# Kernel tuning notes

Measured on AMD Instinct MI355X. Metric: run time of the kernel, lower is better.

## Reference

```python
import jax, jax.numpy as jnp
import numpy as np

E = 1024
H = 16
D = E // H  # projection_dim = 64


def setup_inputs() -> dict:
    key = jax.random.key(0)
    ks = jax.random.split(key, 9)
    s = 1.0 / np.sqrt(E)
    return {
        "inputs": jax.random.normal(ks[0], (2, 2048, E), dtype=jnp.float32),
        "Wq": jax.random.uniform(ks[1], (E, E), jnp.float32, -s, s),
        "bq": jax.random.uniform(ks[2], (E,), jnp.float32, -s, s),
        "Wk": jax.random.uniform(ks[3], (E, E), jnp.float32, -s, s),
        "bk": jax.random.uniform(ks[4], (E,), jnp.float32, -s, s),
        "Wv": jax.random.uniform(ks[5], (E, E), jnp.float32, -s, s),
        "bv": jax.random.uniform(ks[6], (E,), jnp.float32, -s, s),
        "Wo": jax.random.uniform(ks[7], (E, E), jnp.float32, -s, s),
        "bo": jax.random.uniform(ks[8], (E,), jnp.float32, -s, s),
    }


def reference(inputs, Wq, bq, Wk, bk, Wv, bv, Wo, bo):
    B, S, _ = inputs.shape
    # Linear layers use y = x @ W.T + b (torch convention); weights here stored as [E,E]
    q = inputs @ Wq.T + bq
    k = inputs @ Wk.T + bk
    v = inputs @ Wv.T + bv
    # separate heads: [B,S,E] -> [B,H,S,D]
    q = q.reshape(B, S, H, D).transpose(0, 2, 1, 3)
    k = k.reshape(B, S, H, D).transpose(0, 2, 1, 3)
    v = v.reshape(B, S, H, D).transpose(0, 2, 1, 3)
    scale = 1.0 / jnp.sqrt(jnp.float32(D))
    scores = jnp.einsum('bhqd,bhkd->bhqk', q, k) * scale  # [B,H,S,S]
    weights = jax.nn.softmax(scores, axis=-1)
    attn = jnp.einsum('bhqk,bhkd->bhqd', weights, v)  # [B,H,S,D]
    concat = attn.transpose(0, 2, 1, 3).reshape(B, S, E)
    # dropout is identity in eval mode
    return concat @ Wo.T + bo
```

## Files before the change

kernel.cpp:

```cpp
#include <hip/hip_runtime.h>
#include <hip/hip_bf16.h>
#include <stdint.h>

#define E_ 1024
#define H_ 16
#define D_ 64
#define B_ 2
#define S_ 2048
#define M_ 4096

typedef __bf16 bf16_t;
typedef __bf16 bf16x8 __attribute__((ext_vector_type(8)));
typedef __bf16 bf16x4 __attribute__((ext_vector_type(4)));
typedef __bf16 bf16x2 __attribute__((ext_vector_type(2)));
typedef float  f32x4  __attribute__((ext_vector_type(4)));
typedef float  f32x16 __attribute__((ext_vector_type(16)));
typedef unsigned int u32x2 __attribute__((ext_vector_type(2)));
typedef unsigned int u32x4 __attribute__((ext_vector_type(4)));

__global__ __launch_bounds__(256) void cvt_all(
    const float* __restrict__ x,
    const float* __restrict__ w0, const float* __restrict__ w1,
    const float* __restrict__ w2, const float* __restrict__ w3,
    bf16_t* __restrict__ xd,
    bf16_t* __restrict__ d0, bf16_t* __restrict__ d1,
    bf16_t* __restrict__ d2, bf16_t* __restrict__ d3) {
  int i = blockIdx.x * blockDim.x + threadIdx.x;
  const float* src;
  bf16_t* dst;
  int off;
  if (i < (1 << 20)) {
    src = x; dst = xd; off = i;
  } else {
    int j = i - (1 << 20);
    int z = j >> 18;
    off = j & ((1 << 18) - 1);
    src = (z == 0) ? w0 : (z == 1) ? w1 : (z == 2) ? w2 : w3;
    dst = (z == 0) ? d0 : (z == 1) ? d1 : (z == 2) ? d2 : d3;
  }
  float4 v = reinterpret_cast<const float4*>(src)[off];
  bf16x4 o;
  o[0] = (bf16_t)v.x; o[1] = (bf16_t)v.y; o[2] = (bf16_t)v.z; o[3] = (bf16_t)v.w;
  reinterpret_cast<bf16x4*>(dst)[off] = o;
}

static __device__ __forceinline__ void gl_lds16(const bf16_t* g, bf16_t* l) {
  __builtin_amdgcn_global_load_lds((__attribute__((address_space(1))) void*)g,
                                   (__attribute__((address_space(3))) void*)l,
                                   16, 0, 0);
}

template <int SWAP>
static __device__ __forceinline__ void gemm128_mainloop(
    const bf16_t* __restrict__ Ag, const bf16_t* __restrict__ Bg,
    bf16_t* ldsA0, bf16_t* ldsA1, bf16_t* ldsB0, bf16_t* ldsB1,
    int m0, int n0, f32x4 acc[4][4]) {
  const int tid  = threadIdx.x;
  const int lane = tid & 63, wave = tid >> 6;
  const int lrow = lane & 15, lgrp = lane >> 4;
  const int wr = (wave >> 1) * 64, wc = (wave & 1) * 64;
  const int skol = (lane & 3) * 8;
  const int c0 = wave * 2;
  const int rowA = c0 * 16 + (lane >> 2);
  const f32x4 zero = {0.f, 0.f, 0.f, 0.f};
#pragma unroll
  for (int i = 0; i < 4; i++)
#pragma unroll
    for (int j = 0; j < 4; j++) acc[i][j] = zero;

  gl_lds16(Ag + (size_t)(m0 + rowA) * E_ + skol,      ldsA0 + c0 * 512);
  gl_lds16(Ag + (size_t)(m0 + rowA + 16) * E_ + skol, ldsA0 + (c0 + 1) * 512);
  gl_lds16(Bg + (size_t)(n0 + rowA) * E_ + skol,      ldsB0 + c0 * 512);
  gl_lds16(Bg + (size_t)(n0 + rowA + 16) * E_ + skol, ldsB0 + (c0 + 1) * 512);
  __syncthreads();

  for (int kt = 0; kt < E_ / 32; ++kt) {
    bf16_t* sA = (kt & 1) ? ldsA1 : ldsA0;
    bf16_t* sB = (kt & 1) ? ldsB1 : ldsB0;
    if (kt + 1 < E_ / 32) {
      bf16_t* dA = (kt & 1) ? ldsA0 : ldsA1;
      bf16_t* dB = (kt & 1) ? ldsB0 : ldsB1;
      const int k0 = (kt + 1) * 32;
      gl_lds16(Ag + (size_t)(m0 + rowA) * E_ + k0 + skol,      dA + c0 * 512);
      gl_lds16(Ag + (size_t)(m0 + rowA + 16) * E_ + k0 + skol, dA + (c0 + 1) * 512);
      gl_lds16(Bg + (size_t)(n0 + rowA) * E_ + k0 + skol,      dB + c0 * 512);
      gl_lds16(Bg + (size_t)(n0 + rowA + 16) * E_ + k0 + skol, dB + (c0 + 1) * 512);
    }
    bf16x8 fA[4], fB[4];
#pragma unroll
    for (int i = 0; i < 4; i++)
      fA[i] = *reinterpret_cast<const bf16x8*>(sA + (wr + i * 16 + lrow) * 32 + lgrp * 8);
#pragma unroll
    for (int j = 0; j < 4; j++)
      fB[j] = *reinterpret_cast<const bf16x8*>(sB + (wc + j * 16 + lrow) * 32 + lgrp * 8);
#pragma unroll
    for (int i = 0; i < 4; i++)
#pragma unroll
      for (int j = 0; j < 4; j++)
        acc[i][j] = SWAP
          ? __builtin_amdgcn_mfma_f32_16x16x32_bf16(fB[j], fA[i], acc[i][j], 0, 0, 0)
          : __builtin_amdgcn_mfma_f32_16x16x32_bf16(fA[i], fB[j], acc[i][j], 0, 0, 0);
    __syncthreads();
  }
}

__global__ __launch_bounds__(256) void qkv_gemm(
    const bf16_t* __restrict__ xbf, const bf16_t* __restrict__ Wqkv,
    const float* __restrict__ bq, const float* __restrict__ bk, const float* __restrict__ bv,
    bf16_t* __restrict__ Qo, bf16_t* __restrict__ Ko, bf16_t* __restrict__ Vt) {
  __shared__ alignas(16) bf16_t ldsA[2][128 * 32];
  __shared__ alignas(16) bf16_t ldsB[2][128 * 32];
  const int m0 = blockIdx.x * 128, n0 = blockIdx.y * 128;
  const int z = n0 >> 10;
  const float* bias = (z == 0) ? bq : ((z == 1) ? bk : bv);
  const int lane = threadIdx.x & 63, wave = threadIdx.x >> 6;
  const int lrow = lane & 15, lgrp = lane >> 4;
  const int wr = (wave >> 1) * 64, wc = (wave & 1) * 64;
  f32x4 acc[4][4];

  if (z == 2) {
    gemm128_mainloop<0>(xbf, Wqkv, ldsA[0], ldsA[1], ldsB[0], ldsB[1], m0, n0, acc);
#pragma unroll
    for (int i = 0; i < 4; i++) {
      const int mbase = m0 + wr + i * 16 + lgrp * 4;
      const int b = mbase >> 11, s = mbase & (S_ - 1);
#pragma unroll
      for (int j = 0; j < 4; j++) {
        const int nl = (n0 & 1023) + wc + j * 16 + lrow;
        const float bn = bias[nl];
        const int h = nl >> 6, d = nl & 63;
        bf16x4 v;
#pragma unroll
        for (int r = 0; r < 4; r++) v[r] = (bf16_t)(acc[i][j][r] + bn);
        *reinterpret_cast<bf16x4*>(Vt + ((size_t)((b * H_ + h) * D_ + d)) * S_ + s) = v;
      }
    }
  } else {
    gemm128_mainloop<1>(xbf, Wqkv, ldsA[0], ldsA[1], ldsB[0], ldsB[1], m0, n0, acc);
    bf16_t* O = (z == 0) ? Qo : Ko;
    const float scale = (z == 0) ? 0.18033688011112042f : 1.0f;
#pragma unroll
    for (int i = 0; i < 4; i++) {
      const int m = m0 + wr + i * 16 + lrow;
      const int b = m >> 11, s = m & (S_ - 1);
#pragma unroll
      for (int j = 0; j < 4; j++) {
        const int nb = (n0 & 1023) + wc + j * 16 + lgrp * 4;
        const int h = nb >> 6, d = nb & 63;
        const f32x4 b4 = *reinterpret_cast<const f32x4*>(bias + nb);
        bf16x4 v;
#pragma unroll
        for (int r = 0; r < 4; r++) v[r] = (bf16_t)((acc[i][j][r] + b4[r]) * scale);
        *reinterpret_cast<bf16x4*>(O + ((size_t)((b * H_ + h) * S_) + s) * D_ + d) = v;
      }
    }
  }
}

__global__ __launch_bounds__(256) void out_gemm(
    const bf16_t* __restrict__ Cbf, const bf16_t* __restrict__ Wob,
    const float* __restrict__ bo, float* __restrict__ out) {
  __shared__ alignas(16) bf16_t ldsA[2][128 * 32];
  __shared__ alignas(16) bf16_t ldsB[2][128 * 32];
  const int m0 = blockIdx.x * 128, n0 = blockIdx.y * 128;
  f32x4 acc[4][4];
  gemm128_mainloop<1>(Cbf, Wob, ldsA[0], ldsA[1], ldsB[0], ldsB[1], m0, n0, acc);

  const int lane = threadIdx.x & 63, wave = threadIdx.x >> 6;
  const int lrow = lane & 15, lgrp = lane >> 4;
  const int wr = (wave >> 1) * 64, wc = (wave & 1) * 64;
#pragma unroll
  for (int i = 0; i < 4; i++) {
    const int m = m0 + wr + i * 16 + lrow;
#pragma unroll
    for (int j = 0; j < 4; j++) {
      const int nb = n0 + wc + j * 16 + lgrp * 4;
      const f32x4 b4 = *reinterpret_cast<const f32x4*>(bo + nb);
      f32x4 v = acc[i][j] + b4;
      *reinterpret_cast<f32x4*>(out + (size_t)m * E_ + nb) = v;
    }
  }
}


static __device__ __forceinline__ unsigned pack2(float a, float b) {
  bf16x2 t; t[0] = (bf16_t)a; t[1] = (bf16_t)b;
  return __builtin_bit_cast(unsigned, t);
}

static __device__ __forceinline__ bf16x8 mkfrag(unsigned a0, unsigned a1,
                                                unsigned a2, unsigned a3) {
  u32x2 s02 = __builtin_amdgcn_permlane32_swap(a0, a2, false, false);
  u32x2 s13 = __builtin_amdgcn_permlane32_swap(a1, a3, false, false);
  u32x4 t; t[0] = s02[0]; t[1] = s13[0]; t[2] = s02[1]; t[3] = s13[1];
  return *reinterpret_cast<bf16x8*>(&t);
}

__global__ __launch_bounds__(512) void attn_kernel(
    const bf16_t* __restrict__ Qg, const bf16_t* __restrict__ Kg,
    const bf16_t* __restrict__ Vtg, bf16_t* __restrict__ Og) {
  __shared__ alignas(16) bf16_t Kl[2][2][64 * 64];
  __shared__ alignas(16) bf16_t Vl[2][2][64 * 64];
  const int f = blockIdx.x;
  const int bh = (f & 7) * 4 + (f >> 7);
  const int q0 = ((f >> 3) & 15) * 128;
  const int tid = threadIdx.x, lane = tid & 63, wave = tid >> 6;
  const int qsub = wave & 3, kvg = wave >> 2;
  const int ql = lane & 31, hi = lane >> 5;
  const bf16_t* Qb = Qg + (size_t)bh * S_ * D_;
  const bf16_t* Kb = Kg + (size_t)bh * S_ * D_;
  const bf16_t* Vb = Vtg + (size_t)bh * D_ * S_;

  const int q = q0 + qsub * 32 + ql;
  bf16x8 qf[4];
#pragma unroll
  for (int ds = 0; ds < 4; ds++)
    qf[ds] = *reinterpret_cast<const bf16x8*>(Qb + (size_t)q * D_ + ds * 16 + hi * 8);

  f32x16 o0, o1;
#pragma unroll
  for (int r = 0; r < 16; r++) { o0[r] = 0.f; o1[r] = 0.f; }
  float li = 0.f;

  const int srow_lo = lane >> 3;
  const int sunit = lane & 7;

#pragma unroll
  for (int p = 0; p < 2; p++) {
    int c = p * 4 + qsub;
    int row = c * 8 + srow_lo;
    int u = sunit ^ (row & 7);
    gl_lds16(Kb + (size_t)(kvg * 64 + row) * D_ + u * 8, &Kl[kvg][0][c * 512]);
    gl_lds16(Vb + (size_t)row * S_ + kvg * 64 + u * 8, &Vl[kvg][0][c * 512]);
  }
  __syncthreads();

  for (int it = 0; it < S_ / 128; ++it) {
    const int cur = it & 1;
    if (it + 1 < S_ / 128) {
      const int kvn = (kvg + (it + 1) * 2) * 64;
#pragma unroll
      for (int p = 0; p < 2; p++) {
        int c = p * 4 + qsub;
        int row = c * 8 + srow_lo;
        int u = sunit ^ (row & 7);
        gl_lds16(Kb + (size_t)(kvn + row) * D_ + u * 8, &Kl[kvg][cur ^ 1][c * 512]);
        gl_lds16(Vb + (size_t)row * S_ + kvn + u * 8, &Vl[kvg][cur ^ 1][c * 512]);
      }
    }
    const char* kbuf = reinterpret_cast<const char*>(&Kl[kvg][cur][0]);
    const char* vbuf = reinterpret_cast<const char*>(&Vl[kvg][cur][0]);

    f32x16 pa0, pa1;
#pragma unroll
    for (int r = 0; r < 16; r++) { pa0[r] = 0.f; pa1[r] = 0.f; }
    __builtin_amdgcn_s_setprio(1);
#pragma unroll
    for (int ds = 0; ds < 4; ds++) {
      {
        const int krow = ql;
        const int u = (ds * 2 + hi) ^ (krow & 7);
        bf16x8 kf = *reinterpret_cast<const bf16x8*>(kbuf + krow * 128 + u * 16);
        pa0 = __builtin_amdgcn_mfma_f32_32x32x16_bf16(kf, qf[ds], pa0, 0, 0, 0);
      }
      {
        const int krow = 32 + ql;
        const int u = (ds * 2 + hi) ^ (krow & 7);
        bf16x8 kf = *reinterpret_cast<const bf16x8*>(kbuf + krow * 128 + u * 16);
        pa1 = __builtin_amdgcn_mfma_f32_32x32x16_bf16(kf, qf[ds], pa1, 0, 0, 0);
      }
    }
    __builtin_amdgcn_s_setprio(0);

#pragma unroll
    for (int r = 0; r < 16; r++) {
      pa0[r] = __builtin_amdgcn_exp2f(pa0[r]);
      pa1[r] = __builtin_amdgcn_exp2f(pa1[r]);
    }
    float s8[8];
#pragma unroll
    for (int i = 0; i < 8; i++)
      s8[i] = (pa0[2 * i] + pa0[2 * i + 1]) + (pa1[2 * i] + pa1[2 * i + 1]);
    float s4a = s8[0] + s8[1], s4b = s8[2] + s8[3];
    float s4c = s8[4] + s8[5], s4d = s8[6] + s8[7];
    float ps = (s4a + s4b) + (s4c + s4d);
    {
      u32x2 ss = __builtin_amdgcn_permlane32_swap(
          __builtin_bit_cast(unsigned, ps), __builtin_bit_cast(unsigned, ps), false, false);
      ps = __builtin_bit_cast(float, ss[0]) + __builtin_bit_cast(float, ss[1]);
    }
    li += ps;

    unsigned w0[8], w1[8];
#pragma unroll
    for (int i = 0; i < 8; i++) {
      w0[i] = pack2(pa0[2 * i], pa0[2 * i + 1]);
      w1[i] = pack2(pa1[2 * i], pa1[2 * i + 1]);
    }
    bf16x8 bfr[4];
    bfr[0] = mkfrag(w0[0], w0[1], w0[2], w0[3]);
    bfr[1] = mkfrag(w0[4], w0[5], w0[6], w0[7]);
    bfr[2] = mkfrag(w1[0], w1[1], w1[2], w1[3]);
    bfr[3] = mkfrag(w1[4], w1[5], w1[6], w1[7]);

    __builtin_amdgcn_s_setprio(1);
#pragma unroll
    for (int step = 0; step < 4; step++) {
      {
        const int vrow = ql;
        const int u = (step * 2 + hi) ^ (vrow & 7);
        bf16x8 vf = *reinterpret_cast<const bf16x8*>(vbuf + vrow * 128 + u * 16);
        o0 = __builtin_amdgcn_mfma_f32_32x32x16_bf16(vf, bfr[step], o0, 0, 0, 0);
      }
      {
        const int vrow = 32 + ql;
        const int u = (step * 2 + hi) ^ (vrow & 7);
        bf16x8 vf = *reinterpret_cast<const bf16x8*>(vbuf + vrow * 128 + u * 16);
        o1 = __builtin_amdgcn_mfma_f32_32x32x16_bf16(vf, bfr[step], o1, 0, 0, 0);
      }
    }
    __builtin_amdgcn_s_setprio(0);

    __syncthreads();
  }

  f32x4* smO = reinterpret_cast<f32x4*>(&Kl[0][0][0]);
  float* smL = reinterpret_cast<float*>(&Vl[0][0][0]);
  const int mi_ = qsub * 64 + lane;
  if (kvg == 1) {
#pragma unroll
    for (int g = 0; g < 4; g++) {
      f32x4 a;
#pragma unroll
      for (int i = 0; i < 4; i++) a[i] = o0[g * 4 + i];
      smO[g * 256 + mi_] = a;
    }
#pragma unroll
    for (int g = 0; g < 4; g++) {
      f32x4 a;
#pragma unroll
      for (int i = 0; i < 4; i++) a[i] = o1[g * 4 + i];
      smO[(g + 4) * 256 + mi_] = a;
    }
    smL[mi_] = li;
  }
  __syncthreads();
  if (kvg == 0) {
    li += smL[mi_];
#pragma unroll
    for (int g = 0; g < 4; g++) {
      f32x4 a = smO[g * 256 + mi_];
#pragma unroll
      for (int i = 0; i < 4; i++) o0[g * 4 + i] += a[i];
    }
#pragma unroll
    for (int g = 0; g < 4; g++) {
      f32x4 a = smO[(g + 4) * 256 + mi_];
#pragma unroll
      for (int i = 0; i < 4; i++) o1[g * 4 + i] += a[i];
    }
    const float inv = 1.0f / li;
    const int b = bh >> 4, h = bh & 15;
    bf16_t* orow = Og + (size_t)(b * S_ + q) * E_ + h * 64;
#pragma unroll
    for (int g = 0; g < 4; g++) {
      bf16x4 v;
#pragma unroll
      for (int i = 0; i < 4; i++) v[i] = (bf16_t)(o0[g * 4 + i] * inv);
      *reinterpret_cast<bf16x4*>(orow + g * 8 + hi * 4) = v;
    }
#pragma unroll
    for (int g = 0; g < 4; g++) {
      bf16x4 v;
#pragma unroll
      for (int i = 0; i < 4; i++) v[i] = (bf16_t)(o1[g * 4 + i] * inv);
      *reinterpret_cast<bf16x4*>(orow + 32 + g * 8 + hi * 4) = v;
    }
  }
}

extern "C" void kernel_launch(void* const* d_in, const int* in_sizes, int n_in,
                              void* d_out, int out_size, void* d_ws, size_t ws_size,
                              hipStream_t stream) {
  (void)in_sizes; (void)n_in; (void)out_size; (void)ws_size;
  const float* x  = (const float*)d_in[0];
  const float* Wq = (const float*)d_in[1];
  const float* bq = (const float*)d_in[2];
  const float* Wk = (const float*)d_in[3];
  const float* bk = (const float*)d_in[4];
  const float* Wv = (const float*)d_in[5];
  const float* bv = (const float*)d_in[6];
  const float* Wo = (const float*)d_in[7];
  const float* bo = (const float*)d_in[8];
  float* out = (float*)d_out;

  bf16_t* ws  = (bf16_t*)d_ws;
  bf16_t* xbf = ws;
  bf16_t* Ct  = ws;
  bf16_t* wqb = ws + (4u << 20);
  bf16_t* wkb = ws + (5u << 20);
  bf16_t* wvb = ws + (6u << 20);
  bf16_t* wob = ws + (7u << 20);
  bf16_t* Qt  = ws + (8u << 20);
  bf16_t* Kt  = ws + (12u << 20);
  bf16_t* Vt  = ws + (16u << 20);

  cvt_all<<<8192, 256, 0, stream>>>(x, Wq, Wk, Wv, Wo, xbf, wqb, wkb, wvb, wob);

  qkv_gemm<<<dim3(32, 24), 256, 0, stream>>>(xbf, wqb, bq, bk, bv, Qt, Kt, Vt);
  attn_kernel<<<512, 512, 0, stream>>>(Qt, Kt, Vt, Ct);
  out_gemm<<<dim3(32, 8), 256, 0, stream>>>(Ct, wob, bo, out);
}
```

Baseline: 128.2 us.

## Store K/V in MFMA-fragment order and load directly from global, dropping LDS staging

The QKV GEMM epilogue now writes K and V in a pre-swizzled per-lane fragment layout, so the attention kernel can load each MFMA operand with one coalesced 16-byte global load per lane. This removes the LDS double buffer, the async global-to-LDS copies and the per-iteration block barrier in the attention loop. The cost is that K/V tiles are re-read from global/L2 by every wave without shared reuse and without explicit prefetch, so the loop becomes more sensitive to memory latency. The row-sum reduction is also folded into the exp loop.

```diff
diff --git a/kernel.cpp b/kernel.cpp
--- a/kernel.cpp
+++ b/kernel.cpp
@@ -107,7 +107,7 @@
 __global__ __launch_bounds__(256) void qkv_gemm(
     const bf16_t* __restrict__ xbf, const bf16_t* __restrict__ Wqkv,
     const float* __restrict__ bq, const float* __restrict__ bk, const float* __restrict__ bv,
-    bf16_t* __restrict__ Qo, bf16_t* __restrict__ Ko, bf16_t* __restrict__ Vt) {
+    bf16_t* __restrict__ Qo, bf16_t* __restrict__ Kf, bf16_t* __restrict__ Vf) {
   __shared__ alignas(16) bf16_t ldsA[2][128 * 32];
   __shared__ alignas(16) bf16_t ldsB[2][128 * 32];
   const int m0 = blockIdx.x * 128, n0 = blockIdx.y * 128;
@@ -123,22 +123,45 @@
 #pragma unroll
     for (int i = 0; i < 4; i++) {
       const int mbase = m0 + wr + i * 16 + lgrp * 4;
-      const int b = mbase >> 11, s = mbase & (S_ - 1);
+      const int b = mbase >> 11, kv = mbase & (S_ - 1);
+      const int t = kv >> 6, st = (kv >> 4) & 3, hi2 = (kv >> 3) & 1, j0 = kv & 7;
 #pragma unroll
       for (int j = 0; j < 4; j++) {
-        const int nl = (n0 & 1023) + wc + j * 16 + lrow;
-        const float bn = bias[nl];
-        const int h = nl >> 6, d = nl & 63;
+        const int n = (n0 & 1023) + wc + j * 16 + lrow;
+        const float bn = bias[n];
+        const int h = n >> 6, d = n & 63;
+        const int hh = d >> 5, lane2 = (hi2 << 5) | (d & 31);
         bf16x4 v;
 #pragma unroll
         for (int r = 0; r < 4; r++) v[r] = (bf16_t)(acc[i][j][r] + bn);
-        *reinterpret_cast<bf16x4*>(Vt + ((size_t)((b * H_ + h) * D_ + d)) * S_ + s) = v;
+        const size_t off = ((((size_t)(b * H_ + h) * 32 + t) * 8 + hh * 4 + st) * 64 + lane2) * 8 + j0;
+        *reinterpret_cast<bf16x4*>(Vf + off) = v;
+      }
+    }
+  } else if (z == 1) {
+    gemm128_mainloop<1>(xbf, Wqkv, ldsA[0], ldsA[1], ldsB[0], ldsB[1], m0, n0, acc);
+#pragma unroll
+    for (int i = 0; i < 4; i++) {
+      const int m = m0 + wr + i * 16 + lrow;
+      const int b = m >> 11, kv = m & (S_ - 1);
+      const int t = kv >> 6, hh = (kv >> 5) & 1, qll = kv & 31;
+#pragma unroll
+      for (int j = 0; j < 4; j++) {
+        const int nb = (n0 & 1023) + wc + j * 16 + lgrp * 4;
+        const int h = nb >> 6, d = nb & 63;
+        const int ds = d >> 4, hi2 = (d >> 3) & 1, el = d & 7;
+        const int lane2 = (hi2 << 5) | qll;
+        const f32x4 b4 = *reinterpret_cast<const f32x4*>(bias + nb);
+        bf16x4 v;
+#pragma unroll
+        for (int r = 0; r < 4; r++) v[r] = (bf16_t)(acc[i][j][r] + b4[r]);
+        const size_t off = ((((size_t)(b * H_ + h) * 32 + t) * 8 + hh * 4 + ds) * 64 + lane2) * 8 + el;
+        *reinterpret_cast<bf16x4*>(Kf + off) = v;
       }
     }
   } else {
     gemm128_mainloop<1>(xbf, Wqkv, ldsA[0], ldsA[1], ldsB[0], ldsB[1], m0, n0, acc);
-    bf16_t* O = (z == 0) ? Qo : Ko;
-    const float scale = (z == 0) ? 0.18033688011112042f : 1.0f;
+    const float scale = 0.18033688011112042f;
 #pragma unroll
     for (int i = 0; i < 4; i++) {
       const int m = m0 + wr + i * 16 + lrow;
@@ -151,7 +174,7 @@
         bf16x4 v;
 #pragma unroll
         for (int r = 0; r < 4; r++) v[r] = (bf16_t)((acc[i][j][r] + b4[r]) * scale);
-        *reinterpret_cast<bf16x4*>(O + ((size_t)((b * H_ + h) * S_) + s) * D_ + d) = v;
+        *reinterpret_cast<bf16x4*>(Qo + ((size_t)((b * H_ + h) * S_) + s) * D_ + d) = v;
       }
     }
   }
@@ -197,10 +220,10 @@
 }
 
 __global__ __launch_bounds__(512) void attn_kernel(
-    const bf16_t* __restrict__ Qg, const bf16_t* __restrict__ Kg,
-    const bf16_t* __restrict__ Vtg, bf16_t* __restrict__ Og) {
-  __shared__ alignas(16) bf16_t Kl[2][2][64 * 64];
-  __shared__ alignas(16) bf16_t Vl[2][2][64 * 64];
+    const bf16_t* __restrict__ Qg, const bf16_t* __restrict__ Kfg,
+    const bf16_t* __restrict__ Vfg, bf16_t* __restrict__ Og) {
+  __shared__ alignas(16) f32x4 smO[8 * 256];
+  __shared__ float smL[256];
   const int f = blockIdx.x;
   const int bh = (f & 7) * 4 + (f >> 7);
   const int q0 = ((f >> 3) & 15) * 128;
@@ -208,8 +231,8 @@
   const int qsub = wave & 3, kvg = wave >> 2;
   const int ql = lane & 31, hi = lane >> 5;
   const bf16_t* Qb = Qg + (size_t)bh * S_ * D_;
-  const bf16_t* Kb = Kg + (size_t)bh * S_ * D_;
-  const bf16_t* Vb = Vtg + (size_t)bh * D_ * S_;
+  const bf16x8* Kb = reinterpret_cast<const bf16x8*>(Kfg) + (size_t)bh * 32 * 512 + lane;
+  const bf16x8* Vb = reinterpret_cast<const bf16x8*>(Vfg) + (size_t)bh * 32 * 512 + lane;
 
   const int q = q0 + qsub * 32 + ql;
   bf16x8 qf[4];
@@ -222,34 +245,14 @@
   for (int r = 0; r < 16; r++) { o0[r] = 0.f; o1[r] = 0.f; }
   float li = 0.f;
 
-  const int srow_lo = lane >> 3;
-  const int sunit = lane & 7;
-
-#pragma unroll
-  for (int p = 0; p < 2; p++) {
-    int c = p * 4 + qsub;
-    int row = c * 8 + srow_lo;
-    int u = sunit ^ (row & 7);
-    gl_lds16(Kb + (size_t)(kvg * 64 + row) * D_ + u * 8, &Kl[kvg][0][c * 512]);
-    gl_lds16(Vb + (size_t)row * S_ + kvg * 64 + u * 8, &Vl[kvg][0][c * 512]);
-  }
-  __syncthreads();
-
   for (int it = 0; it < S_ / 128; ++it) {
-    const int cur = it & 1;
-    if (it + 1 < S_ / 128) {
-      const int kvn = (kvg + (it + 1) * 2) * 64;
-#pragma unroll
-      for (int p = 0; p < 2; p++) {
-        int c = p * 4 + qsub;
-        int row = c * 8 + srow_lo;
-        int u = sunit ^ (row & 7);
-        gl_lds16(Kb + (size_t)(kvn + row) * D_ + u * 8, &Kl[kvg][cur ^ 1][c * 512]);
-        gl_lds16(Vb + (size_t)row * S_ + kvn + u * 8, &Vl[kvg][cur ^ 1][c * 512]);
-      }
-    }
-    const char* kbuf = reinterpret_cast<const char*>(&Kl[kvg][cur][0]);
-    const char* vbuf = reinterpret_cast<const char*>(&Vl[kvg][cur][0]);
+    const int t = kvg + it * 2;
+    const bf16x8* kt = Kb + (size_t)t * 512;
+    const bf16x8* vt = Vb + (size_t)t * 512;
+
+    bf16x8 kf0[4], kf1[4];
+#pragma unroll
+    for (int ds = 0; ds < 4; ds++) { kf0[ds] = kt[ds * 64]; kf1[ds] = kt[(4 + ds) * 64]; }
 
     f32x16 pa0, pa1;
 #pragma unroll
@@ -257,33 +260,21 @@
     __builtin_amdgcn_s_setprio(1);
 #pragma unroll
     for (int ds = 0; ds < 4; ds++) {
-      {
-        const int krow = ql;
-        const int u = (ds * 2 + hi) ^ (krow & 7);
-        bf16x8 kf = *reinterpret_cast<const bf16x8*>(kbuf + krow * 128 + u * 16);
-        pa0 = __builtin_amdgcn_mfma_f32_32x32x16_bf16(kf, qf[ds], pa0, 0, 0, 0);
-      }
-      {
-        const int krow = 32 + ql;
-        const int u = (ds * 2 + hi) ^ (krow & 7);
-        bf16x8 kf = *reinterpret_cast<const bf16x8*>(kbuf + krow * 128 + u * 16);
-        pa1 = __builtin_amdgcn_mfma_f32_32x32x16_bf16(kf, qf[ds], pa1, 0, 0, 0);
-      }
+      pa0 = __builtin_amdgcn_mfma_f32_32x32x16_bf16(kf0[ds], qf[ds], pa0, 0, 0, 0);
+      pa1 = __builtin_amdgcn_mfma_f32_32x32x16_bf16(kf1[ds], qf[ds], pa1, 0, 0, 0);
     }
     __builtin_amdgcn_s_setprio(0);
 
+    bf16x8 vf0[4], vf1[4];
+#pragma unroll
+    for (int st = 0; st < 4; st++) { vf0[st] = vt[st * 64]; vf1[st] = vt[(4 + st) * 64]; }
+
+    float ps = 0.f;
 #pragma unroll
     for (int r = 0; r < 16; r++) {
-      pa0[r] = __builtin_amdgcn_exp2f(pa0[r]);
-      pa1[r] = __builtin_amdgcn_exp2f(pa1[r]);
-    }
-    float s8[8];
-#pragma unroll
-    for (int i = 0; i < 8; i++)
-      s8[i] = (pa0[2 * i] + pa0[2 * i + 1]) + (pa1[2 * i] + pa1[2 * i + 1]);
-    float s4a = s8[0] + s8[1], s4b = s8[2] + s8[3];
-    float s4c = s8[4] + s8[5], s4d = s8[6] + s8[7];
-    float ps = (s4a + s4b) + (s4c + s4d);
+      pa0[r] = __builtin_amdgcn_exp2f(pa0[r]); ps += pa0[r];
+      pa1[r] = __builtin_amdgcn_exp2f(pa1[r]); ps += pa1[r];
+    }
     {
       u32x2 ss = __builtin_amdgcn_permlane32_swap(
           __builtin_bit_cast(unsigned, ps), __builtin_bit_cast(unsigned, ps), false, false);
@@ -305,27 +296,13 @@
 
     __builtin_amdgcn_s_setprio(1);
 #pragma unroll
-    for (int step = 0; step < 4; step++) {
-      {
-        const int vrow = ql;
-        const int u = (step * 2 + hi) ^ (vrow & 7);
-        bf16x8 vf = *reinterpret_cast<const bf16x8*>(vbuf + vrow * 128 + u * 16);
-        o0 = __builtin_amdgcn_mfma_f32_32x32x16_bf16(vf, bfr[step], o0, 0, 0, 0);
-      }
-      {
-        const int vrow = 32 + ql;
-        const int u = (step * 2 + hi) ^ (vrow & 7);
-        bf16x8 vf = *reinterpret_cast<const bf16x8*>(vbuf + vrow * 128 + u * 16);
-        o1 = __builtin_amdgcn_mfma_f32_32x32x16_bf16(vf, bfr[step], o1, 0, 0, 0);
-      }
+    for (int st = 0; st < 4; st++) {
+      o0 = __builtin_amdgcn_mfma_f32_32x32x16_bf16(vf0[st], bfr[st], o0, 0, 0, 0);
+      o1 = __builtin_amdgcn_mfma_f32_32x32x16_bf16(vf1[st], bfr[st], o1, 0, 0, 0);
     }
     __builtin_amdgcn_s_setprio(0);
-
-    __syncthreads();
-  }
-
-  f32x4* smO = reinterpret_cast<f32x4*>(&Kl[0][0][0]);
-  float* smL = reinterpret_cast<float*>(&Vl[0][0][0]);
+  }
+
   const int mi_ = qsub * 64 + lane;
   if (kvg == 1) {
 #pragma unroll
@@ -402,12 +379,12 @@
   bf16_t* wvb = ws + (6u << 20);
   bf16_t* wob = ws + (7u << 20);
   bf16_t* Qt  = ws + (8u << 20);
-  bf16_t* Kt  = ws + (12u << 20);
-  bf16_t* Vt  = ws + (16u << 20);
+  bf16_t* Kf  = ws + (12u << 20);
+  bf16_t* Vf  = ws + (16u << 20);
 
   cvt_all<<<8192, 256, 0, stream>>>(x, Wq, Wk, Wv, Wo, xbf, wqb, wkb, wvb, wob);
 
-  qkv_gemm<<<dim3(32, 24), 256, 0, stream>>>(xbf, wqb, bq, bk, bv, Qt, Kt, Vt);
-  attn_kernel<<<512, 512, 0, stream>>>(Qt, Kt, Vt, Ct);
+  qkv_gemm<<<dim3(32, 24), 256, 0, stream>>>(xbf, wqb, bq, bk, bv, Qt, Kf, Vf);
+  attn_kernel<<<512, 512, 0, stream>>>(Qt, Kf, Vf, Ct);
   out_gemm<<<dim3(32, 8), 256, 0, stream>>>(Ct, wob, bo, out);
 }
```

New measurement: 115.3 us. 10.0% less time.
